# Kernel tuning notes

Hardware: AMD Instinct MI355X
Metric: run time of the kernel (lower is better)

## Reference

```python
import jax, jax.numpy as jnp
import numpy as np

N_NODES = 100000
N_EDGES = 1600000
IN_CH = 128
OUT_CH = 128
N_REL = 64
N_BASES = 8


def setup_inputs() -> dict:
    key = jax.random.key(0)
    k = jax.random.split(key, 7)
    x = jax.random.normal(k[0], (N_NODES, IN_CH), dtype=jnp.float32)
    src = jax.random.randint(k[1], (N_EDGES,), 0, N_NODES, dtype=jnp.int32)
    rel = jax.random.randint(k[2], (N_EDGES,), 0, N_REL, dtype=jnp.int32)
    dst = jax.random.randint(k[3], (N_EDGES,), 0, N_NODES, dtype=jnp.int32)
    edge_triples = jnp.stack([src, rel, dst], axis=1)  # [E, 3] (src, rel, dst)
    # xavier-uniform-ish scales
    basis = jax.random.normal(k[4], (N_BASES, IN_CH, OUT_CH), dtype=jnp.float32) * (2.0 / (IN_CH + OUT_CH)) ** 0.5
    att = jax.random.normal(k[5], (N_REL, N_BASES), dtype=jnp.float32) * (2.0 / (N_REL + N_BASES)) ** 0.5
    root_w = jax.random.normal(k[6], (IN_CH, OUT_CH), dtype=jnp.float32) * (1.0 / IN_CH) ** 0.5
    root_b = jnp.zeros((OUT_CH,), dtype=jnp.float32)
    return {"x": x, "edge_triples": edge_triples, "num_nodes": N_NODES,
            "basis": basis, "att": att, "root_w": root_w, "root_b": root_b}


def reference(x, edge_triples, num_nodes, basis, att, root_w, root_b):
    src = edge_triples[:, 0]
    rel = edge_triples[:, 1]
    dst = edge_triples[:, 2]
    att_e = att[rel]  # [E, B]
    n_bases = basis.shape[0]
    e = src.shape[0]
    out_ch = basis.shape[2]
    # messages[e] = x[src[e]] @ (sum_b att[rel[e], b] * basis[b])
    # computed as sum_b att_e[:, b] * (x @ basis[b])[src] to avoid the huge
    # per-edge [E, in, out] weight gather the torch code materializes.
    msgs = jnp.zeros((e, out_ch), dtype=x.dtype)
    for b in range(n_bases):  # small fixed loop over bases
        yb = x @ basis[b]  # [N, out]
        msgs = msgs + att_e[:, b:b + 1] * yb[src]
    # degree normalization (mean aggregation over incoming edges)
    deg = jax.ops.segment_sum(jnp.ones((e,), dtype=x.dtype), dst, num_segments=num_nodes)
    deg_inv = jnp.where(deg > 0, 1.0 / deg, 0.0)
    msgs = msgs * deg_inv[dst][:, None]
    agg = jax.ops.segment_sum(msgs, dst, num_segments=num_nodes)  # [N, out]
    return agg + x @ root_w + root_b
```

## Files before the change

kernel.cpp:

```cpp
#include <hip/hip_runtime.h>

#define NCH 128
#define NREL 64
#define NBP 1024
#define ESB 4096
#define CAPF 3072
#define CAPH 2048
#define KTOT 1152
#define KST 36
#define ZROW 2304

typedef __attribute__((ext_vector_type(8))) short bf16x8;
typedef __attribute__((ext_vector_type(4))) float f32x4;
typedef __attribute__((ext_vector_type(2))) float f32x2;

__device__ __forceinline__ unsigned short f2bf(float f) {
    unsigned u = __float_as_uint(f);
    return (unsigned short)((u + 0x7fffu + ((u >> 16) & 1u)) >> 16);
}
__device__ __forceinline__ unsigned pack2bf(float a, float b) {
    return (unsigned)f2bf(a) | ((unsigned)f2bf(b) << 16);
}

__global__ __launch_bounds__(256) void k_prep(const float* __restrict__ x,
                                              unsigned short* __restrict__ x_bf,
                                              long total8) {
    long i = (long)blockIdx.x * 256 + threadIdx.x;
    if (i >= total8) return;
    const float4* xp = (const float4*)x;
    float4 v0 = xp[i * 2], v1 = xp[i * 2 + 1];
    bf16x8 p;
    p[0] = (short)f2bf(v0.x); p[1] = (short)f2bf(v0.y);
    p[2] = (short)f2bf(v0.z); p[3] = (short)f2bf(v0.w);
    p[4] = (short)f2bf(v1.x); p[5] = (short)f2bf(v1.y);
    p[6] = (short)f2bf(v1.z); p[7] = (short)f2bf(v1.w);
    ((bf16x8*)x_bf)[i] = p;
}

__global__ __launch_bounds__(256) void k_buildB(const float* __restrict__ basis,
                                                const float* __restrict__ att,
                                                const float* __restrict__ rw,
                                                float* __restrict__ attc,
                                                unsigned short* __restrict__ basisP) {
    int idx = blockIdx.x * 256 + threadIdx.x;
    if (idx < 512) attc[idx] = att[idx];
    if (idx >= 128 * KTOT) return;
    int j = idx & 7, lg = (idx >> 3) & 3, oc = (idx >> 5) & 127, kk = idx >> 12;
    int k = kk * 32 + lg * 8 + j;
    float v = (k < 1024) ? basis[(size_t)(k >> 7) * NCH * NCH + (size_t)(k & 127) * NCH + oc]
                         : rw[(size_t)(k - 1024) * NCH + oc];
    basisP[idx] = f2bf(v);
}

__global__ __launch_bounds__(256) void k_count(const int* __restrict__ trip, int E, int NB,
                                               int* __restrict__ cntB) {
    __shared__ int hb[NBP];
    int t = threadIdx.x;
    for (int i = t; i < NB; i += 256) hb[i] = 0;
    __syncthreads();
    int base = blockIdx.x * ESB;
#pragma unroll
    for (int i = 0; i < ESB / 256; ++i) {
        int e = base + i * 256 + t;
        if (e < E) atomicAdd(&hb[trip[3 * e + 2] >> 7], 1);
    }
    __syncthreads();
    for (int i = t; i < NB; i += 256) cntB[(size_t)blockIdx.x * NB + i] = hb[i];
}

__global__ __launch_bounds__(1024) void k_scanB(int* __restrict__ cntB, int GB, int NB,
                                                int* __restrict__ bhist) {
    __shared__ int sc[1024];
    int t = threadIdx.x, b = blockIdx.x;
    int v = (t < GB) ? cntB[(size_t)t * NB + b] : 0;
    sc[t] = v;
    __syncthreads();
    for (int off = 1; off < 1024; off <<= 1) {
        int a = (t >= off) ? sc[t - off] : 0;
        __syncthreads();
        sc[t] += a;
        __syncthreads();
    }
    if (t < GB) cntB[(size_t)t * NB + b] = sc[t] - v;
    if (t == GB - 1) bhist[b] = sc[t];
}

__global__ __launch_bounds__(1024) void k_offsets(const int* __restrict__ bhist, int NB,
                                                  int* __restrict__ bucketoff) {
    __shared__ int sc[1024];
    int t = threadIdx.x;
    int d = (t < NB) ? bhist[t] : 0;
    sc[t] = d;
    __syncthreads();
    for (int off = 1; off < 1024; off <<= 1) {
        int a = (t >= off) ? sc[t - off] : 0;
        __syncthreads();
        sc[t] += a;
        __syncthreads();
    }
    if (t < NB) bucketoff[t] = sc[t] - d;
    if (t == NB - 1) bucketoff[NB] = sc[t];
}

__global__ __launch_bounds__(256) void k_scatter(const int* __restrict__ trip, int E, int NB,
                                                 const int* __restrict__ cntB,
                                                 const int* __restrict__ bucketoff,
                                                 unsigned* __restrict__ packed) {
    __shared__ int cb[NBP], lbase[NBP], delta[NBP];
    __shared__ int ssc[256];
    __shared__ unsigned lpk[ESB];
    __shared__ unsigned short lb[ESB];
    int t = threadIdx.x, blk = blockIdx.x;
    for (int i = t; i < NB; i += 256) cb[i] = 0;
    __syncthreads();
    int base = blk * ESB;
    int total = min(ESB, E - base);

    unsigned pk[ESB / 256];
    int rk[ESB / 256];
    unsigned short bk[ESB / 256];
#pragma unroll
    for (int i = 0; i < ESB / 256; ++i) {
        int e = base + i * 256 + t;
        pk[i] = 0; rk[i] = 0; bk[i] = 0;
        if (e < E) {
            int src = trip[3 * e], rel = trip[3 * e + 1], dst = trip[3 * e + 2];
            int bkt = dst >> 7;
            bk[i] = (unsigned short)bkt;
            pk[i] = ((unsigned)(dst & 127) << 23) | ((unsigned)rel << 17) | (unsigned)src;
            rk[i] = atomicAdd(&cb[bkt], 1);
        }
    }
    __syncthreads();
    int ch = (NB + 255) >> 8;
    int mysum = 0;
    for (int i = 0; i < ch; ++i) {
        int idx = t * ch + i;
        if (idx < NB) mysum += cb[idx];
    }
    ssc[t] = mysum;
    __syncthreads();
    for (int off = 1; off < 256; off <<= 1) {
        int a = (t >= off) ? ssc[t - off] : 0;
        __syncthreads();
        ssc[t] += a;
        __syncthreads();
    }
    int run = ssc[t] - mysum;
    for (int i = 0; i < ch; ++i) {
        int idx = t * ch + i;
        if (idx < NB) { lbase[idx] = run; run += cb[idx]; }
    }
    __syncthreads();
    for (int i = t; i < NB; i += 256)
        delta[i] = bucketoff[i] + cntB[(size_t)blk * NB + i] - lbase[i];
    __syncthreads();
#pragma unroll
    for (int i = 0; i < ESB / 256; ++i) {
        int e = base + i * 256 + t;
        if (e < E) {
            int j = lbase[bk[i]] + rk[i];
            lpk[j] = pk[i];
            lb[j] = bk[i];
        }
    }
    __syncthreads();
    for (int j = t; j < total; j += 256)
        packed[delta[lb[j]] + j] = lpk[j];
}

__global__ __launch_bounds__(256) void k_sortbkt(const unsigned* __restrict__ packed,
                                                 const int* __restrict__ bucketoff,
                                                 unsigned* __restrict__ sortedG,
                                                 int* __restrict__ dstoffG) {
    __shared__ int h[128], hs[128];
    int t = threadIdx.x, b = blockIdx.x;
    if (t < 128) h[t] = 0;
    __syncthreads();
    int s0 = bucketoff[b], s1 = bucketoff[b + 1];
    int cnt = min(s1 - s0, CAPF);

    unsigned pk[CAPF / 256];
    int rk[CAPF / 256];
#pragma unroll
    for (int i = 0; i < CAPF / 256; ++i) {
        int j = i * 256 + t;
        pk[i] = 0; rk[i] = 0;
        if (j < cnt) {
            unsigned p = packed[s0 + j];
            pk[i] = p;
            rk[i] = atomicAdd(&h[p >> 23], 1);
        }
    }
    __syncthreads();
    if (t < 128) hs[t] = h[t];
    __syncthreads();
    for (int off = 1; off < 128; off <<= 1) {
        int a = (t < 128 && t >= off) ? hs[t - off] : 0;
        __syncthreads();
        if (t < 128) hs[t] += a;
        __syncthreads();
    }
    if (t < 128) dstoffG[b * 129 + t] = hs[t] - h[t];
    if (t == 0) dstoffG[b * 129 + 128] = cnt;
#pragma unroll
    for (int i = 0; i < CAPF / 256; ++i) {
        int j = i * 256 + t;
        if (j < cnt) {
            int d = pk[i] >> 23;
            sortedG[s0 + hs[d] - h[d] + rk[i]] = pk[i];
        }
    }
}

__global__ __launch_bounds__(512, 4) void k_fused(const unsigned* __restrict__ x32,
                                                  const unsigned* __restrict__ sortedG,
                                                  const int* __restrict__ bucketoff,
                                                  const int* __restrict__ dstoffG,
                                                  const float* __restrict__ attc,
                                                  const unsigned short* __restrict__ basisP,
                                                  const float* __restrict__ rb,
                                                  float* __restrict__ out, int N) {
    __shared__ bf16x8 ztV[16 * (ZROW / 16)];
    __shared__ unsigned sortedE[CAPH];
    __shared__ f32x2 attp[512];
    __shared__ int doffsL[65];
    __shared__ int nextD;
    char* zt = (char*)ztV;

    int t = threadIdx.x;
    int bucket = blockIdx.x >> 1, half = blockIdx.x & 1;
    int w = t >> 6, lane = t & 63, lr = lane & 15, lg = lane >> 4;
    int nb0 = bucket * 128 + half * 64;

    if (t < 512) { float v = attc[t]; attp[t] = (f32x2){v, v}; }
    int rawIdx = bucket * 129 + half * 64;
    int rawBase = dstoffG[rawIdx];
    int cnt = min(dstoffG[rawIdx + 64] - rawBase, CAPH);
    if (t < 65) doffsL[t] = min(dstoffG[rawIdx + t] - rawBase, CAPH);
    if (t == 0) nextD = 0;
    int sG0 = bucketoff[bucket] + rawBase;
    for (int j = t; j < cnt; j += 512) {
        unsigned p = sortedG[sG0 + j];
        sortedE[j] = (((p >> 17) & 63u) << 26) | ((p & 0x1FFFFu) << 8);
    }
    __syncthreads();

    const char* xb = (const char*)x32 + lane * 4;

    f32x2 z[8];
#pragma unroll
    for (int i = 0; i < 8; ++i) z[i] = (f32x2){0.f, 0.f};

    for (int r = 0; r < 4; ++r) {
        int rEnd = r * 16 + 16;

        auto FLUSH = [&](int d, int cnt_d) {
            float inv = (cnt_d > 0) ? 1.f / (float)cnt_d : 0.f;
            int zr = d & 15;
            char* zrow = zt + zr * ZROW;
            int sw = zr & 7;
#pragma unroll
            for (int bb = 0; bb < 8; ++bb) {
                unsigned pq = pack2bf(z[bb].x * inv, z[bb].y * inv);
                int unit = (bb * 16 + (lane >> 2)) ^ sw;
                *(unsigned*)(zrow + (unit << 4) + ((lane & 3) << 2)) = pq;
                z[bb] = (f32x2){0.f, 0.f};
            }
            int n = nb0 + d;
            unsigned xv = (n < N) ? x32[(size_t)n * 64 + lane] : 0u;
            int unit = (128 + (lane >> 2)) ^ sw;
            *(unsigned*)(zrow + (unit << 4) + ((lane & 3) << 2)) = xv;
        };

        for (;;) {
            int my = 0x7FFFFFFF;
            if (lane == 0) my = atomicAdd(&nextD, 1);
            my = __shfl(my, 0, 64);
            if (my >= rEnd) break;
            int d = my;
            int eBeg = doffsL[d], eEnd = doffsL[d + 1];
            int cnt_d = eEnd - eBeg;

            if (cnt_d > 0) {
                int last = eEnd - 1;
                unsigned xvA[8], xvB[8], xvC[8];
                unsigned relA = 0, relB = 0, relC = 0;
                unsigned long long rlA = 0, rlB = 0, rlC = 0;

                auto LOAD8 = [&](unsigned* xvX, unsigned long long& relX, int base2) {
                    unsigned pk8[8];
                    if (base2 + 7 <= last) {
#pragma unroll
                        for (int i = 0; i < 8; ++i) pk8[i] = sortedE[base2 + i];
                    } else {
#pragma unroll
                        for (int i = 0; i < 8; ++i) pk8[i] = sortedE[min(base2 + i, last)];
                    }
                    unsigned long long rp = 0;
#pragma unroll
                    for (int i = 0; i < 8; ++i) {
                        rp |= (unsigned long long)(pk8[i] >> 26) << (6 * i);
                        xvX[i] = *(const unsigned*)(xb + (pk8[i] & 0x03FFFF00u));
                    }
                    relX = rp;
                };
                auto CONSUME8 = [&](const unsigned* xvX, unsigned long long relX, int base2) {
#pragma unroll
                    for (int i = 0; i < 8; ++i) {
                        int e = base2 + i;
                        if (e < eEnd) {
                            const f32x2* ap = &attp[((unsigned)(relX >> (6 * i)) & 63u) * 8];
                            unsigned xv = xvX[i];
                            f32x2 vlh;
                            vlh.x = __uint_as_float(xv << 16);
                            vlh.y = __uint_as_float(xv & 0xffff0000u);
                            z[0] += ap[0] * vlh;
                            z[1] += ap[1] * vlh;
                            z[2] += ap[2] * vlh;
                            z[3] += ap[3] * vlh;
                            z[4] += ap[4] * vlh;
                            z[5] += ap[5] * vlh;
                            z[6] += ap[6] * vlh;
                            z[7] += ap[7] * vlh;
                        }
                    }
                };

                LOAD8(xvA, rlA, eBeg);
                LOAD8(xvB, rlB, eBeg + 8);
                LOAD8(xvC, rlC, eBeg + 16);
                for (int e0 = eBeg; e0 < eEnd; e0 += 24) {
                    CONSUME8(xvA, rlA, e0);
                    if (e0 + 24 < eEnd) LOAD8(xvA, rlA, e0 + 24);
                    CONSUME8(xvB, rlB, e0 + 8);
                    if (e0 + 32 < eEnd) LOAD8(xvB, rlB, e0 + 32);
                    CONSUME8(xvC, rlC, e0 + 16);
                    if (e0 + 40 < eEnd) LOAD8(xvC, rlC, e0 + 40);
                }
                (void)relA; (void)relB; (void)relC;
            }
            FLUSH(d, cnt_d);
        }
        __syncthreads();

        f32x4 acc = {0.f, 0.f, 0.f, 0.f};
        int ocr = w * 16 + lr;
        int sw = lr & 7;
#pragma unroll 6
        for (int kk = 0; kk < KST; ++kk) {
            bf16x8 a = *(const bf16x8*)(zt + lr * ZROW + ((((kk << 2) + lg) ^ sw) << 4));
            bf16x8 b0 = *(const bf16x8*)(basisP + ((((size_t)kk * 128 + ocr) * 4 + lg) << 3));
            acc = __builtin_amdgcn_mfma_f32_16x16x32_bf16(b0, a, acc, 0, 0, 0);
        }

        int n = nb0 + r * 16 + lr;
        if (n < N) {
            int oc0 = w * 16 + lg * 4;
            f32x4 bias = *(const f32x4*)(rb + oc0);
            *(f32x4*)(out + (size_t)n * NCH + oc0) = acc + bias;
        }
        if (t == 0) nextD = rEnd;
        __syncthreads();
    }
}

extern "C" void kernel_launch(void* const* d_in, const int* in_sizes, int n_in,
                              void* d_out, int out_size, void* d_ws, size_t ws_size,
                              hipStream_t stream) {
    const float* x = (const float*)d_in[0];
    const int* trip = (const int*)d_in[1];
    const float* basis = (const float*)d_in[3];
    const float* att = (const float*)d_in[4];
    const float* rw = (const float*)d_in[5];
    const float* rb = (const float*)d_in[6];
    float* out = (float*)d_out;

    int N = in_sizes[0] / NCH;
    int E = in_sizes[1] / 3;
    int NB = (N + 127) >> 7;
    int GB = (E + ESB - 1) / ESB;

    char* ws = (char*)d_ws;
    size_t off = 0;
    auto alloc = [&](size_t bts) { size_t o = off; off = (off + bts + 255) & ~(size_t)255; return o; };
    size_t oXbf    = alloc((size_t)N * NCH * 2);
    size_t oBasisP = alloc((size_t)128 * KTOT * 2);
    size_t oAttc   = alloc(512 * 4);
    size_t oCntB   = alloc((size_t)GB * NB * 4);
    size_t oBhist  = alloc((NBP + 1) * 4);
    size_t oBktoff = alloc((NBP + 1) * 4);
    size_t oPacked = alloc((size_t)E * 4);
    size_t oSorted = alloc((size_t)E * 4);
    size_t oDoff   = alloc((size_t)NB * 129 * 4);
    (void)off; (void)ws_size;

    unsigned short* x_bf = (unsigned short*)(ws + oXbf);
    unsigned short* basisP = (unsigned short*)(ws + oBasisP);
    float* attc = (float*)(ws + oAttc);
    int* cntB = (int*)(ws + oCntB);
    int* bhist = (int*)(ws + oBhist);
    int* bucketoff = (int*)(ws + oBktoff);
    unsigned* packed = (unsigned*)(ws + oPacked);
    unsigned* sortedG = (unsigned*)(ws + oSorted);
    int* dstoffG = (int*)(ws + oDoff);

    long total8 = (long)N * NCH / 8;
    k_prep<<<(int)((total8 + 255) / 256), 256, 0, stream>>>(x, x_bf, total8);
    k_buildB<<<(128 * KTOT + 255) / 256, 256, 0, stream>>>(basis, att, rw, attc, basisP);
    k_count<<<GB, 256, 0, stream>>>(trip, E, NB, cntB);
    k_scanB<<<NB, 1024, 0, stream>>>(cntB, GB, NB, bhist);
    k_offsets<<<1, 1024, 0, stream>>>(bhist, NB, bucketoff);
    k_scatter<<<GB, 256, 0, stream>>>(trip, E, NB, cntB, bucketoff, packed);
    k_sortbkt<<<NB, 256, 0, stream>>>(packed, bucketoff, sortedG, dstoffG);
    k_fused<<<NB * 2, 512, 0, stream>>>((const unsigned*)x_bf, sortedG, bucketoff, dstoffG,
                                        attc, basisP, rb, out, N);
}
```

Measured before the change: 290.5 us.

## Compute per-node basis-weighted edge aggregation with MFMA instead of scalar FMAs

The per-destination aggregation of att[rel]*x[src] over edges becomes a small matrix product. Each wave builds a 16x32 attention fragment and 32x128 gathered-x fragments per chunk of 32 edges and runs eight bf16 MFMAs into 8x128 accumulators. The z-buffer layout and basis packing order switch from basis-major to channel-major (k = ch*8 + b) to match. The aim is to move the inner multiply-add work onto the matrix units. In exchange, gathers become scalar 16-bit loads (eight per edge per lane), padded rows waste MFMA work for low-degree nodes, and attention is now rounded to bf16.

```diff
diff --git a/kernel.cpp b/kernel.cpp
--- a/kernel.cpp
+++ b/kernel.cpp
@@ -12,7 +12,6 @@
 
 typedef __attribute__((ext_vector_type(8))) short bf16x8;
 typedef __attribute__((ext_vector_type(4))) float f32x4;
-typedef __attribute__((ext_vector_type(2))) float f32x2;
 
 __device__ __forceinline__ unsigned short f2bf(float f) {
     unsigned u = __float_as_uint(f);
@@ -40,15 +39,23 @@
 __global__ __launch_bounds__(256) void k_buildB(const float* __restrict__ basis,
                                                 const float* __restrict__ att,
                                                 const float* __restrict__ rw,
-                                                float* __restrict__ attc,
+                                                unsigned short* __restrict__ attB,
                                                 unsigned short* __restrict__ basisP) {
     int idx = blockIdx.x * 256 + threadIdx.x;
-    if (idx < 512) attc[idx] = att[idx];
+    if (idx < 1040) {
+        int rr = idx >> 4, b = idx & 15;
+        attB[idx] = (rr < NREL && b < 8) ? f2bf(att[rr * 8 + b]) : (unsigned short)0;
+    }
     if (idx >= 128 * KTOT) return;
     int j = idx & 7, lg = (idx >> 3) & 3, oc = (idx >> 5) & 127, kk = idx >> 12;
     int k = kk * 32 + lg * 8 + j;
-    float v = (k < 1024) ? basis[(size_t)(k >> 7) * NCH * NCH + (size_t)(k & 127) * NCH + oc]
-                         : rw[(size_t)(k - 1024) * NCH + oc];
+    float v;
+    if (k < 1024) {
+        int b = k & 7, ch = k >> 3;
+        v = basis[(size_t)b * NCH * NCH + (size_t)ch * NCH + oc];
+    } else {
+        v = rw[(size_t)(k - 1024) * NCH + oc];
+    }
     basisP[idx] = f2bf(v);
 }
 
@@ -214,16 +221,17 @@
 }
 
 __global__ __launch_bounds__(512, 4) void k_fused(const unsigned* __restrict__ x32,
+                                                  const unsigned short* __restrict__ xus,
                                                   const unsigned* __restrict__ sortedG,
                                                   const int* __restrict__ bucketoff,
                                                   const int* __restrict__ dstoffG,
-                                                  const float* __restrict__ attc,
+                                                  const unsigned short* __restrict__ attBg,
                                                   const unsigned short* __restrict__ basisP,
                                                   const float* __restrict__ rb,
                                                   float* __restrict__ out, int N) {
     __shared__ bf16x8 ztV[16 * (ZROW / 16)];
     __shared__ unsigned sortedE[CAPH];
-    __shared__ f32x2 attp[512];
+    __shared__ unsigned short attl[1056];
     __shared__ int doffsL[65];
     __shared__ int nextD;
     char* zt = (char*)ztV;
@@ -231,9 +239,10 @@
     int t = threadIdx.x;
     int bucket = blockIdx.x >> 1, half = blockIdx.x & 1;
     int w = t >> 6, lane = t & 63, lr = lane & 15, lg = lane >> 4;
+    int l15 = lane & 15;
     int nb0 = bucket * 128 + half * 64;
 
-    if (t < 512) { float v = attc[t]; attp[t] = (f32x2){v, v}; }
+    for (int i = t; i < 1040; i += 512) attl[i] = attBg[i];
     int rawIdx = bucket * 129 + half * 64;
     int rawBase = dstoffG[rawIdx];
     int cnt = min(dstoffG[rawIdx + 64] - rawBase, CAPH);
@@ -246,32 +255,8 @@
     }
     __syncthreads();
 
-    const char* xb = (const char*)x32 + lane * 4;
-
-    f32x2 z[8];
-#pragma unroll
-    for (int i = 0; i < 8; ++i) z[i] = (f32x2){0.f, 0.f};
-
     for (int r = 0; r < 4; ++r) {
         int rEnd = r * 16 + 16;
-
-        auto FLUSH = [&](int d, int cnt_d) {
-            float inv = (cnt_d > 0) ? 1.f / (float)cnt_d : 0.f;
-            int zr = d & 15;
-            char* zrow = zt + zr * ZROW;
-            int sw = zr & 7;
-#pragma unroll
-            for (int bb = 0; bb < 8; ++bb) {
-                unsigned pq = pack2bf(z[bb].x * inv, z[bb].y * inv);
-                int unit = (bb * 16 + (lane >> 2)) ^ sw;
-                *(unsigned*)(zrow + (unit << 4) + ((lane & 3) << 2)) = pq;
-                z[bb] = (f32x2){0.f, 0.f};
-            }
-            int n = nb0 + d;
-            unsigned xv = (n < N) ? x32[(size_t)n * 64 + lane] : 0u;
-            int unit = (128 + (lane >> 2)) ^ sw;
-            *(unsigned*)(zrow + (unit << 4) + ((lane & 3) << 2)) = xv;
-        };
 
         for (;;) {
             int my = 0x7FFFFFFF;
@@ -281,84 +266,72 @@
             int d = my;
             int eBeg = doffsL[d], eEnd = doffsL[d + 1];
             int cnt_d = eEnd - eBeg;
-
-            if (cnt_d > 0) {
-                int last = eEnd - 1;
-                unsigned xvA[8], xvB[8], xvC[8];
-                unsigned relA = 0, relB = 0, relC = 0;
-                unsigned long long rlA = 0, rlB = 0, rlC = 0;
-
-                auto LOAD8 = [&](unsigned* xvX, unsigned long long& relX, int base2) {
-                    unsigned pk8[8];
-                    if (base2 + 7 <= last) {
-#pragma unroll
-                        for (int i = 0; i < 8; ++i) pk8[i] = sortedE[base2 + i];
-                    } else {
-#pragma unroll
-                        for (int i = 0; i < 8; ++i) pk8[i] = sortedE[min(base2 + i, last)];
-                    }
-                    unsigned long long rp = 0;
-#pragma unroll
-                    for (int i = 0; i < 8; ++i) {
-                        rp |= (unsigned long long)(pk8[i] >> 26) << (6 * i);
-                        xvX[i] = *(const unsigned*)(xb + (pk8[i] & 0x03FFFF00u));
-                    }
-                    relX = rp;
-                };
-                auto CONSUME8 = [&](const unsigned* xvX, unsigned long long relX, int base2) {
-#pragma unroll
-                    for (int i = 0; i < 8; ++i) {
-                        int e = base2 + i;
-                        if (e < eEnd) {
-                            const f32x2* ap = &attp[((unsigned)(relX >> (6 * i)) & 63u) * 8];
-                            unsigned xv = xvX[i];
-                            f32x2 vlh;
-                            vlh.x = __uint_as_float(xv << 16);
-                            vlh.y = __uint_as_float(xv & 0xffff0000u);
-                            z[0] += ap[0] * vlh;
-                            z[1] += ap[1] * vlh;
-                            z[2] += ap[2] * vlh;
-                            z[3] += ap[3] * vlh;
-                            z[4] += ap[4] * vlh;
-                            z[5] += ap[5] * vlh;
-                            z[6] += ap[6] * vlh;
-                            z[7] += ap[7] * vlh;
-                        }
-                    }
-                };
-
-                LOAD8(xvA, rlA, eBeg);
-                LOAD8(xvB, rlB, eBeg + 8);
-                LOAD8(xvC, rlC, eBeg + 16);
-                for (int e0 = eBeg; e0 < eEnd; e0 += 24) {
-                    CONSUME8(xvA, rlA, e0);
-                    if (e0 + 24 < eEnd) LOAD8(xvA, rlA, e0 + 24);
-                    CONSUME8(xvB, rlB, e0 + 8);
-                    if (e0 + 32 < eEnd) LOAD8(xvB, rlB, e0 + 32);
-                    CONSUME8(xvC, rlC, e0 + 16);
-                    if (e0 + 40 < eEnd) LOAD8(xvC, rlC, e0 + 40);
+            int n = nb0 + d;
+            unsigned xv = (n < N) ? x32[(size_t)n * 64 + lane] : 0u;
+
+            f32x4 acc[8];
+#pragma unroll
+            for (int nt = 0; nt < 8; ++nt) acc[nt] = (f32x4){0.f, 0.f, 0.f, 0.f};
+
+            int last = eEnd - 1;
+            for (int c0 = eBeg; c0 < eEnd; c0 += 32) {
+                int kb = c0 + (lg << 3);
+                bf16x8 aF;
+                bf16x8 bF[8];
+#pragma unroll
+                for (int j = 0; j < 8; ++j) {
+                    int e = kb + j;
+                    unsigned ew = sortedE[min(e, last)];
+                    int arow = (e < eEnd) ? (int)(ew >> 26) : 64;
+                    aF[j] = (short)attl[arow * 16 + l15];
+                    unsigned xi = ((ew & 0x03FFFF00u) >> 1) + (unsigned)l15;
+                    bF[0][j] = (short)xus[xi];
+                    bF[1][j] = (short)xus[xi + 16];
+                    bF[2][j] = (short)xus[xi + 32];
+                    bF[3][j] = (short)xus[xi + 48];
+                    bF[4][j] = (short)xus[xi + 64];
+                    bF[5][j] = (short)xus[xi + 80];
+                    bF[6][j] = (short)xus[xi + 96];
+                    bF[7][j] = (short)xus[xi + 112];
                 }
-                (void)relA; (void)relB; (void)relC;
+#pragma unroll
+                for (int nt = 0; nt < 8; ++nt)
+                    acc[nt] = __builtin_amdgcn_mfma_f32_16x16x32_bf16(aF, bF[nt], acc[nt], 0, 0, 0);
             }
-            FLUSH(d, cnt_d);
-        }
-        __syncthreads();
-
-        f32x4 acc = {0.f, 0.f, 0.f, 0.f};
+
+            float inv = (cnt_d > 0) ? 1.f / (float)cnt_d : 0.f;
+            int zr = d & 15, sw = zr & 7;
+            char* zrow = zt + zr * ZROW;
+            if (lane < 32) {
+                int b0 = (lane >> 4) << 2;
+#pragma unroll
+                for (int nt = 0; nt < 8; ++nt) {
+                    int chn = nt * 16 + l15;
+                    uint2 v;
+                    v.x = pack2bf(acc[nt][0] * inv, acc[nt][1] * inv);
+                    v.y = pack2bf(acc[nt][2] * inv, acc[nt][3] * inv);
+                    *(uint2*)(zrow + ((chn ^ sw) << 4) + (b0 << 1)) = v;
+                }
+            }
+            *(unsigned*)(zrow + (((128 + (lane >> 2)) ^ sw) << 4) + ((lane & 3) << 2)) = xv;
+        }
+        __syncthreads();
+
+        f32x4 accM = {0.f, 0.f, 0.f, 0.f};
         int ocr = w * 16 + lr;
-        int sw = lr & 7;
+        int swm = lr & 7;
 #pragma unroll 6
         for (int kk = 0; kk < KST; ++kk) {
-            bf16x8 a = *(const bf16x8*)(zt + lr * ZROW + ((((kk << 2) + lg) ^ sw) << 4));
+            bf16x8 a = *(const bf16x8*)(zt + lr * ZROW + ((((kk << 2) + lg) ^ swm) << 4));
             bf16x8 b0 = *(const bf16x8*)(basisP + ((((size_t)kk * 128 + ocr) * 4 + lg) << 3));
-            acc = __builtin_amdgcn_mfma_f32_16x16x32_bf16(b0, a, acc, 0, 0, 0);
+            accM = __builtin_amdgcn_mfma_f32_16x16x32_bf16(b0, a, accM, 0, 0, 0);
         }
 
         int n = nb0 + r * 16 + lr;
         if (n < N) {
             int oc0 = w * 16 + lg * 4;
             f32x4 bias = *(const f32x4*)(rb + oc0);
-            *(f32x4*)(out + (size_t)n * NCH + oc0) = acc + bias;
+            *(f32x4*)(out + (size_t)n * NCH + oc0) = accM + bias;
         }
         if (t == 0) nextD = rEnd;
         __syncthreads();
@@ -386,7 +359,7 @@
     auto alloc = [&](size_t bts) { size_t o = off; off = (off + bts + 255) & ~(size_t)255; return o; };
     size_t oXbf    = alloc((size_t)N * NCH * 2);
     size_t oBasisP = alloc((size_t)128 * KTOT * 2);
-    size_t oAttc   = alloc(512 * 4);
+    size_t oAttB   = alloc(1056 * 2);
     size_t oCntB   = alloc((size_t)GB * NB * 4);
     size_t oBhist  = alloc((NBP + 1) * 4);
     size_t oBktoff = alloc((NBP + 1) * 4);
@@ -397,7 +370,7 @@
 
     unsigned short* x_bf = (unsigned short*)(ws + oXbf);
     unsigned short* basisP = (unsigned short*)(ws + oBasisP);
-    float* attc = (float*)(ws + oAttc);
+    unsigned short* attB = (unsigned short*)(ws + oAttB);
     int* cntB = (int*)(ws + oCntB);
     int* bhist = (int*)(ws + oBhist);
     int* bucketoff = (int*)(ws + oBktoff);
@@ -407,12 +380,12 @@
 
     long total8 = (long)N * NCH / 8;
     k_prep<<<(int)((total8 + 255) / 256), 256, 0, stream>>>(x, x_bf, total8);
-    k_buildB<<<(128 * KTOT + 255) / 256, 256, 0, stream>>>(basis, att, rw, attc, basisP);
+    k_buildB<<<(128 * KTOT + 255) / 256, 256, 0, stream>>>(basis, att, rw, attB, basisP);
     k_count<<<GB, 256, 0, stream>>>(trip, E, NB, cntB);
     k_scanB<<<NB, 1024, 0, stream>>>(cntB, GB, NB, bhist);
     k_offsets<<<1, 1024, 0, stream>>>(bhist, NB, bucketoff);
     k_scatter<<<GB, 256, 0, stream>>>(trip, E, NB, cntB, bucketoff, packed);
     k_sortbkt<<<NB, 256, 0, stream>>>(packed, bucketoff, sortedG, dstoffG);
-    k_fused<<<NB * 2, 512, 0, stream>>>((const unsigned*)x_bf, sortedG, bucketoff, dstoffG,
-                                        attc, basisP, rb, out, N);
-}
+    k_fused<<<NB * 2, 512, 0, stream>>>((const unsigned*)x_bf, x_bf, sortedG, bucketoff,
+                                        dstoffG, attB, basisP, rb, out, N);
+}
```

Measured after the change: 278.9 us. 4.0% less time.
